# Performance work log

Measured on AMD Instinct MI355X. Metric: run time of the kernel, lower is better.

Reference implementation:

```python
import jax, jax.numpy as jnp
import numpy as np

NH = 32          # nh * 2 neighbors per point (init nh=16)
P_REDUCTION = 0.5


def setup_inputs() -> dict:
    key = jax.random.key(0)
    k1, k2 = jax.random.split(key)
    x = jax.random.normal(k1, (2, 8192, 256), dtype=jnp.float32)       # [b, n, e]
    coords = jax.random.normal(k2, (2, 2, 8192, 1), dtype=jnp.float32) # [b, c, n, 1]
    return {"x": x, "coords": coords}


def _knn_gather(x, coords):
    """Return features of the NH nearest neighbors of each point: [b, n, NH, e]."""
    cs = coords[..., 0]                                   # [b, c, n]
    sq = jnp.sum(cs * cs, axis=1)                         # [b, n]
    # squared euclidean distances [b, n, n]
    d2 = sq[:, :, None] + sq[:, None, :] - 2.0 * jnp.einsum('bcn,bcm->bnm', cs, cs)
    d2 = jax.lax.stop_gradient(d2)                        # indices are non-differentiable
    _, nn_idx = jax.lax.top_k(-d2, NH)                    # [b, n, NH] nearest points
    # gather neighbor features: [b, 1, n, e] indexed with [b, n, NH, 1] -> [b, n, NH, e]
    x_nh = jnp.take_along_axis(x[:, None, :, :], nn_idx[..., None], axis=2)
    return x_nh


def _forward(x, coords):
    b, n, e = x.shape
    x_nh = _knn_gather(x, coords)                         # [b, n, NH, e]
    # unbiased std over the neighbor dim (torch.std default, ddof=1)
    mean_nh = jnp.mean(x_nh, axis=-2, keepdims=True)
    local_s = jnp.sqrt(jnp.sum((x_nh - mean_nh) ** 2, axis=-2) / (NH - 1))  # [b, n, e]
    global_m = jnp.abs(jnp.mean(x, axis=1))               # [b, e]
    local_dist = jnp.sum(local_s / global_m[:, None, :], axis=-1)           # [b, n]
    n_keep = int((1.0 - P_REDUCTION) * n)
    _, keep_idx = jax.lax.top_k(local_dist, n_keep)       # [b, n_keep], sorted desc
    x_out = jnp.take_along_axis(x, keep_idx[:, :, None], axis=1)            # [b, n_keep, e]
    coords_out = jnp.take_along_axis(coords, keep_idx[:, None, :, None], axis=2)  # [b, c, n_keep, 1]
    return x_out, coords_out, local_dist


def reference(x, coords):
    return _forward(x, coords)
```

## Files before the change

### kernel.cpp

```cpp
#include <hip/hip_runtime.h>

#define NN 8192
#define EE 256
#define KNH 32
#define NKEEP 4096
#define NCX 64
#define NCELL 4096
#define CNT_MIN 48

typedef unsigned long long u64;
typedef unsigned int u32;


__device__ __forceinline__ int cellof(float v) {
    const int q = (int)floorf((v + 4.6f) * (64.0f / 9.2f));
    return min(max(q, 0), NCX - 1);
}

__global__ void k_gm_partial(const float* __restrict__ x, float* __restrict__ part) {
    const int b = blockIdx.y, chunk = blockIdx.x, t = threadIdx.x;
    const float* xp = x + ((size_t)b * NN + (size_t)chunk * 256) * EE + t;
    float s = 0.0f;
    for (int i = 0; i < 256; ++i) s += xp[(size_t)i * EE];
    part[((size_t)b * 32 + chunk) * EE + t] = s;
}

__global__ void k_gm_final(const float* __restrict__ part, float* __restrict__ gm) {
    const int b = blockIdx.y, t = threadIdx.x;
    float s = 0.0f;
    for (int c = 0; c < 32; ++c) s += part[((size_t)b * 32 + c) * EE + t];
    gm[b * EE + t] = fabsf(s / (float)NN);
}

__global__ void __launch_bounds__(1024) k_binning(const float* __restrict__ coords,
                                                  int* __restrict__ start,
                                                  float2* __restrict__ sc,
                                                  int* __restrict__ sj) {
    __shared__ int cnt[NCELL];
    __shared__ int ps[1024];
    const int b = blockIdx.x, t = threadIdx.x;
#pragma unroll
    for (int k = 0; k < 4; ++k) cnt[k * 1024 + t] = 0;
    __syncthreads();
#pragma unroll
    for (int k = 0; k < 8; ++k) {
        const int i = k * 1024 + t;
        const float xv = coords[(size_t)b * 2 * NN + i];
        const float yv = coords[(size_t)b * 2 * NN + NN + i];
        atomicAdd(&cnt[cellof(xv) * NCX + cellof(yv)], 1);
    }
    __syncthreads();
    const int v0 = cnt[t * 4 + 0], v1 = cnt[t * 4 + 1];
    const int v2 = cnt[t * 4 + 2], v3 = cnt[t * 4 + 3];
    const int s = v0 + v1 + v2 + v3;
    ps[t] = s;
    __syncthreads();
    for (int d = 1; d < 1024; d <<= 1) {
        const int add = (t >= d) ? ps[t - d] : 0;
        __syncthreads();
        ps[t] += add;
        __syncthreads();
    }
    int run = ps[t] - s;
    start[b * (NCELL + 1) + t * 4 + 0] = run; cnt[t * 4 + 0] = run; run += v0;
    start[b * (NCELL + 1) + t * 4 + 1] = run; cnt[t * 4 + 1] = run; run += v1;
    start[b * (NCELL + 1) + t * 4 + 2] = run; cnt[t * 4 + 2] = run; run += v2;
    start[b * (NCELL + 1) + t * 4 + 3] = run; cnt[t * 4 + 3] = run; run += v3;
    if (t == 0) start[b * (NCELL + 1) + NCELL] = NN;
    __syncthreads();
#pragma unroll
    for (int k = 0; k < 8; ++k) {
        const int i = k * 1024 + t;
        const float xv = coords[(size_t)b * 2 * NN + i];
        const float yv = coords[(size_t)b * 2 * NN + NN + i];
        const int p = atomicAdd(&cnt[cellof(xv) * NCX + cellof(yv)], 1);
        sc[(size_t)b * NN + p] = make_float2(xv, yv);
        sj[(size_t)b * NN + p] = i;
    }
}

__device__ __forceinline__ u64 shfl_xor_u64(u64 v, int m) {
    const u32 hi = (u32)__shfl_xor((int)(u32)(v >> 32), m);
    const u32 lo = (u32)__shfl_xor((int)(u32)v, m);
    return ((u64)hi << 32) | lo;
}

__device__ __forceinline__ u64 wave_min_u64(u64 h) {
#pragma unroll
    for (int s = 1; s < 64; s <<= 1) {
        const u64 o = shfl_xor_u64(h, s);
        h = (o < h) ? o : h;
    }
    return h;
}

__global__ void __launch_bounds__(256) k_knn_dist(
        const float* __restrict__ x,
        const float* __restrict__ gm, const float2* __restrict__ sc,
        const int* __restrict__ sj, const int* __restrict__ start,
        float* __restrict__ ld_out) {
    __shared__ u64 comp[4][64];
    const int wg   = blockIdx.x;
    const int swz  = (wg & 7) * 512 + (wg >> 3);
    const int b    = swz >> 11;
    const int pb   = swz & 2047;
    const int wid  = threadIdx.x >> 6;
    const int lane = threadIdx.x & 63;
    const int p    = pb * 4 + wid;

    const float2* scb = sc + (size_t)b * NN;
    const int*    sjb = sj + (size_t)b * NN;
    const int*    stb = start + b * (NCELL + 1);
    const float2 cp = scb[p];
    const int    i  = sjb[p];
    const float ci0 = cp.x, ci1 = cp.y;
    const int qx = cellof(ci0), qy = cellof(ci1);

    int r = 1, xl, yl, yh, nsl;
    int myc0 = 0, mylen = 0;
    for (;;) {
        xl = max(qx - r, 0);
        const int xh = min(qx + r, NCX - 1);
        yl = max(qy - r, 0);
        yh = min(qy + r, NCX - 1);
        nsl = xh - xl + 1;
        int c0 = 0, c1 = 0;
        if (lane < nsl) {
            c0 = stb[(xl + lane) * NCX + yl];
            c1 = stb[(xl + lane) * NCX + yh + 1];
        }
        myc0 = c0; mylen = c1 - c0;
        int tot = mylen;
#pragma unroll
        for (int s = 1; s < 64; s <<= 1) tot += __shfl_xor(tot, s);
        if (tot >= CNT_MIN || r >= NCX) break;
        r <<= 1;
    }
    int incl = mylen;
#pragma unroll
    for (int d = 1; d < 64; d <<= 1) {
        const int v = __shfl_up(incl, d);
        incl += (lane >= d) ? v : 0;
    }
    int excl = incl - mylen;
    const int L1 = __shfl(incl, 63);

    float dmin = 1e30f;
    for (int g = 0; g < L1; g += 64) {
        const int gp = g + lane;
        int lo = 0, hi = nsl - 1;
#pragma unroll
        for (int st = 0; st < 6; ++st) {
            const int mid = (lo + hi + 1) >> 1;
            const int v = __shfl(excl, mid);
            const bool go = (v <= gp);
            lo = go ? mid : lo;
            hi = go ? hi : mid - 1;
        }
        const int cnd = __shfl(myc0, lo) + gp - __shfl(excl, lo);
        const int cc  = min(max(cnd, 0), NN - 1);
        const float2 pt = scb[cc];
        const float dx = ci0 - pt.x, dy = ci1 - pt.y;
        const float d  = fmaf(dx, dx, dy * dy);
        if (gp < L1) dmin = fminf(dmin, d);
    }

    u32 mk = __float_as_uint(dmin);
#pragma unroll
    for (int k = 2; k <= 64; k <<= 1) {
#pragma unroll
        for (int j = k >> 1; j > 0; j >>= 1) {
            const u32 o = (u32)__shfl_xor((int)mk, j);
            const bool keep_min = (((lane & j) == 0) == ((lane & k) == 0));
            const u32 mn = min(mk, o), mx = max(mk, o);
            mk = keep_min ? mn : mx;
        }
    }
    const u32 T = (u32)__shfl((int)mk, 31);

    const float srad = sqrtf(__uint_as_float(T)) * 1.0002f + 1e-5f;
    xl = cellof(ci0 - srad);
    const int xh2 = cellof(ci0 + srad);
    yl = cellof(ci1 - srad);
    yh = cellof(ci1 + srad);
    nsl = xh2 - xl + 1;
    {
        int c0 = 0, c1 = 0;
        if (lane < nsl) {
            c0 = stb[(xl + lane) * NCX + yl];
            c1 = stb[(xl + lane) * NCX + yh + 1];
        }
        myc0 = c0; mylen = c1 - c0;
    }
    incl = mylen;
#pragma unroll
    for (int d = 1; d < 64; d <<= 1) {
        const int v = __shfl_up(incl, d);
        incl += (lane >= d) ? v : 0;
    }
    excl = incl - mylen;
    const int L2 = __shfl(incl, 63);

    const u64 lmask = (1ull << lane) - 1;
    int base = 0;
    for (int g = 0; g < L2; g += 64) {
        const int gp = g + lane;
        int lo = 0, hi = nsl - 1;
#pragma unroll
        for (int st = 0; st < 6; ++st) {
            const int mid = (lo + hi + 1) >> 1;
            const int v = __shfl(excl, mid);
            const bool go = (v <= gp);
            lo = go ? mid : lo;
            hi = go ? hi : mid - 1;
        }
        const int cnd = __shfl(myc0, lo) + gp - __shfl(excl, lo);
        const int cc  = min(max(cnd, 0), NN - 1);
        const float2 pt = scb[cc];
        const int    jj = sjb[cc];
        const float dx = ci0 - pt.x, dy = ci1 - pt.y;
        const u32 db = __float_as_uint(fmaf(dx, dx, dy * dy));
        const bool keep = (gp < L2) && (db <= T);
        const u64 m = __ballot(keep);
        const int pos = base + __popcll(m & lmask);
        base += __popcll(m);
        if (keep && pos < 64) comp[wid][pos] = ((u64)db << 32) | (u32)jj;
    }
    const bool ovf = (base > 64) || (base < KNH);

    u64 key = (lane < base) ? comp[wid][lane] : ~0ull;
#pragma unroll
    for (int k = 2; k <= 64; k <<= 1) {
#pragma unroll
        for (int j = k >> 1; j > 0; j >>= 1) {
            const u64 other = shfl_xor_u64(key, j);
            const bool keep_min = (((lane & j) == 0) == ((lane & k) == 0));
            const bool lt = (key < other);
            const u64 mn = lt ? key : other;
            const u64 mx = lt ? other : key;
            key = keep_min ? mn : mx;
        }
    }
    int jkeep = (int)(u32)key;

    if (ovf) {
        u64 minkeep = 0;
        for (int k = 0; k < KNH; ++k) {
            u64 best = ~0ull;
            for (int g = 0; g < L2; g += 64) {
                const int gp = g + lane;
                int lo = 0, hi = nsl - 1;
#pragma unroll
                for (int st = 0; st < 6; ++st) {
                    const int mid = (lo + hi + 1) >> 1;
                    const int v = __shfl(excl, mid);
                    const bool go = (v <= gp);
                    lo = go ? mid : lo;
                    hi = go ? hi : mid - 1;
                }
                const int cnd = __shfl(myc0, lo) + gp - __shfl(excl, lo);
                const int cc  = min(max(cnd, 0), NN - 1);
                const float2 pt = scb[cc];
                const int    jj = sjb[cc];
                const float dx = ci0 - pt.x, dy = ci1 - pt.y;
                const float d  = fmaf(dx, dx, dy * dy);
                const u64 kk = ((u64)__float_as_uint(d) << 32) | (u32)jj;
                if (gp < L2 && kk >= minkeep && kk < best) best = kk;
            }
            const u64 h = wave_min_u64(best);
            if (lane == k) jkeep = (int)(u32)h;
            minkeep = h + 1;
        }
    }

    float s1[4] = {0.f, 0.f, 0.f, 0.f};
    float s2[4] = {0.f, 0.f, 0.f, 0.f};
    const float* xb = x + (size_t)b * NN * EE;
#pragma unroll 8
    for (int k = 0; k < KNH; ++k) {
        const int j = __builtin_amdgcn_readlane(jkeep, k);
        const float4 v = *reinterpret_cast<const float4*>(xb + (size_t)j * EE + (lane << 2));
        s1[0] += v.x; s2[0] += v.x * v.x;
        s1[1] += v.y; s2[1] += v.y * v.y;
        s1[2] += v.z; s2[2] += v.z * v.z;
        s1[3] += v.w; s2[3] += v.w * v.w;
    }

    const float* gmb = gm + b * EE;
    float tt = 0.f;
#pragma unroll
    for (int q = 0; q < 4; ++q) {
        const float sum = s1[q];
        float ssd = s2[q] - sum * sum * (1.0f / 32.0f);
        ssd = ssd > 0.f ? ssd : 0.f;
        const float ls = sqrtf(ssd * (1.0f / 31.0f));
        tt += ls / gmb[(lane << 2) + q];
    }
#pragma unroll
    for (int s2r = 1; s2r < 64; s2r <<= 1) tt += __shfl_xor(tt, s2r);

    if (lane == 0) ld_out[(size_t)b * NN + i] = tt;
}

__global__ void k_rank_gather(const float* __restrict__ x, const float* __restrict__ coords,
                              const float* __restrict__ ld,
                              float* __restrict__ x_out, float* __restrict__ c_out) {
    const int b    = blockIdx.y;
    const int wid  = threadIdx.x >> 6;
    const int lane = threadIdx.x & 63;
    const int i    = blockIdx.x * 4 + wid;
    const float* lb = ld + (size_t)b * NN;
    const float di = lb[i];
    int cnt = 0;
    for (int t = 0; t < NN / 64; ++t) {
        const int j = lane + t * 64;
        const float dj = lb[j];
        cnt += (dj > di || (dj == di && j < i)) ? 1 : 0;
    }
#pragma unroll
    for (int s = 1; s < 64; s <<= 1) cnt += __shfl_xor(cnt, s);

    if (cnt < NKEEP) {
        const float4 v = *reinterpret_cast<const float4*>(x + ((size_t)b * NN + i) * EE + (lane << 2));
        *reinterpret_cast<float4*>(x_out + ((size_t)b * NKEEP + cnt) * EE + (lane << 2)) = v;
        if (lane < 2) {
            c_out[((size_t)b * 2 + lane) * NKEEP + cnt] = coords[((size_t)b * 2 + lane) * NN + i];
        }
    }
}

extern "C" void kernel_launch(void* const* d_in, const int* in_sizes, int n_in,
                              void* d_out, int out_size, void* d_ws, size_t ws_size,
                              hipStream_t stream) {
    const float* x      = (const float*)d_in[0];
    const float* coords = (const float*)d_in[1];

    float* out    = (float*)d_out;
    float* x_out  = out;
    float* c_out  = out + 2097152;
    float* ld_out = out + 2113536;

    char*   ws    = (char*)d_ws;
    float*  part  = (float*)(ws);
    float*  gm    = (float*)(ws + 65536);
    int*    start = (int*)  (ws + 67584);
    float2* sc    = (float2*)(ws + 100384);
    int*    sj    = (int*)  (ws + 231456);

    k_binning    <<<2,             1024, 0, stream>>>(coords, start, sc, sj);
    k_gm_partial <<<dim3(32, 2),   256,  0, stream>>>(x, part);
    k_gm_final   <<<dim3(1, 2),    256,  0, stream>>>(part, gm);
    k_knn_dist   <<<4096,          256,  0, stream>>>(x, gm, sc, sj, start, ld_out);
    k_rank_gather<<<dim3(2048, 2), 256,  0, stream>>>(x, coords, ld_out, x_out, c_out);
}
```

Before: 99.04 us.

## Cache candidate distances in LDS, replace bitonic sorts with ballot radix selection

```diff
diff --git a/kernel.cpp b/kernel.cpp
--- a/kernel.cpp
+++ b/kernel.cpp
@@ -7,6 +7,7 @@
 #define NCX 64
 #define NCELL 4096
 #define CNT_MIN 48
+#define CACHE_CAP 512
 
 typedef unsigned long long u64;
 typedef unsigned int u32;
@@ -37,8 +38,9 @@
                                                   float2* __restrict__ sc,
                                                   int* __restrict__ sj) {
     __shared__ int cnt[NCELL];
-    __shared__ int ps[1024];
+    __shared__ int wsum[16];
     const int b = blockIdx.x, t = threadIdx.x;
+    const int lane = t & 63, wv = t >> 6;
 #pragma unroll
     for (int k = 0; k < 4; ++k) cnt[k * 1024 + t] = 0;
     __syncthreads();
@@ -53,15 +55,18 @@
     const int v0 = cnt[t * 4 + 0], v1 = cnt[t * 4 + 1];
     const int v2 = cnt[t * 4 + 2], v3 = cnt[t * 4 + 3];
     const int s = v0 + v1 + v2 + v3;
-    ps[t] = s;
+    int inc = s;
+#pragma unroll
+    for (int d = 1; d < 64; d <<= 1) {
+        const int u = __shfl_up(inc, d);
+        inc += (lane >= d) ? u : 0;
+    }
+    if (lane == 63) wsum[wv] = inc;
     __syncthreads();
-    for (int d = 1; d < 1024; d <<= 1) {
-        const int add = (t >= d) ? ps[t - d] : 0;
-        __syncthreads();
-        ps[t] += add;
-        __syncthreads();
-    }
-    int run = ps[t] - s;
+    int wpre = 0;
+#pragma unroll
+    for (int w = 0; w < 16; ++w) wpre += (w < wv) ? wsum[w] : 0;
+    int run = wpre + inc - s;
     start[b * (NCELL + 1) + t * 4 + 0] = run; cnt[t * 4 + 0] = run; run += v0;
     start[b * (NCELL + 1) + t * 4 + 1] = run; cnt[t * 4 + 1] = run; run += v1;
     start[b * (NCELL + 1) + t * 4 + 2] = run; cnt[t * 4 + 2] = run; run += v2;
@@ -99,6 +104,7 @@
         const float* __restrict__ gm, const float2* __restrict__ sc,
         const int* __restrict__ sj, const int* __restrict__ start,
         float* __restrict__ ld_out) {
+    __shared__ u64 cache[4][CACHE_CAP];
     __shared__ u64 comp[4][64];
     const int wg   = blockIdx.x;
     const int swz  = (wg & 7) * 512 + (wg >> 3);
@@ -116,18 +122,18 @@
     const float ci0 = cp.x, ci1 = cp.y;
     const int qx = cellof(ci0), qy = cellof(ci1);
 
-    int r = 1, xl, yl, yh, nsl;
+    int r = 1, xl1, xh1, yl1, yh1, nsl;
     int myc0 = 0, mylen = 0;
     for (;;) {
-        xl = max(qx - r, 0);
-        const int xh = min(qx + r, NCX - 1);
-        yl = max(qy - r, 0);
-        yh = min(qy + r, NCX - 1);
-        nsl = xh - xl + 1;
+        xl1 = max(qx - r, 0);
+        xh1 = min(qx + r, NCX - 1);
+        yl1 = max(qy - r, 0);
+        yh1 = min(qy + r, NCX - 1);
+        nsl = xh1 - xl1 + 1;
         int c0 = 0, c1 = 0;
         if (lane < nsl) {
-            c0 = stb[(xl + lane) * NCX + yl];
-            c1 = stb[(xl + lane) * NCX + yh + 1];
+            c0 = stb[(xl1 + lane) * NCX + yl1];
+            c1 = stb[(xl1 + lane) * NCX + yh1 + 1];
         }
         myc0 = c0; mylen = c1 - c0;
         int tot = mylen;
@@ -160,105 +166,145 @@
         const int cnd = __shfl(myc0, lo) + gp - __shfl(excl, lo);
         const int cc  = min(max(cnd, 0), NN - 1);
         const float2 pt = scb[cc];
+        const int    jj = sjb[cc];
         const float dx = ci0 - pt.x, dy = ci1 - pt.y;
         const float d  = fmaf(dx, dx, dy * dy);
-        if (gp < L1) dmin = fminf(dmin, d);
-    }
-
-    u32 mk = __float_as_uint(dmin);
-#pragma unroll
-    for (int k = 2; k <= 64; k <<= 1) {
-#pragma unroll
-        for (int j = k >> 1; j > 0; j >>= 1) {
-            const u32 o = (u32)__shfl_xor((int)mk, j);
-            const bool keep_min = (((lane & j) == 0) == ((lane & k) == 0));
-            const u32 mn = min(mk, o), mx = max(mk, o);
-            mk = keep_min ? mn : mx;
-        }
-    }
-    const u32 T = (u32)__shfl((int)mk, 31);
+        if (gp < L1) {
+            dmin = fminf(dmin, d);
+            if (gp < CACHE_CAP) cache[wid][gp] = ((u64)__float_as_uint(d) << 32) | (u32)jj;
+        }
+    }
+
+    const u32 kmin = __float_as_uint(dmin);
+    u32 blo = 0, bhi = 0xFFFFFFFFu;
+    for (int it = 0; it < 32; ++it) {
+        const u32 mid = blo + ((bhi - blo) >> 1);
+        const int c = __popcll(__ballot(kmin <= mid));
+        if (c >= KNH) bhi = mid; else blo = mid + 1;
+    }
+    const u32 T = bhi;
 
     const float srad = sqrtf(__uint_as_float(T)) * 1.0002f + 1e-5f;
-    xl = cellof(ci0 - srad);
-    const int xh2 = cellof(ci0 + srad);
-    yl = cellof(ci1 - srad);
-    yh = cellof(ci1 + srad);
-    nsl = xh2 - xl + 1;
-    {
-        int c0 = 0, c1 = 0;
-        if (lane < nsl) {
-            c0 = stb[(xl + lane) * NCX + yl];
-            c1 = stb[(xl + lane) * NCX + yh + 1];
-        }
-        myc0 = c0; mylen = c1 - c0;
-    }
-    incl = mylen;
-#pragma unroll
-    for (int d = 1; d < 64; d <<= 1) {
-        const int v = __shfl_up(incl, d);
-        incl += (lane >= d) ? v : 0;
-    }
-    excl = incl - mylen;
-    const int L2 = __shfl(incl, 63);
+    const int xl2 = cellof(ci0 - srad), xh2 = cellof(ci0 + srad);
+    const int yl2 = cellof(ci1 - srad), yh2 = cellof(ci1 + srad);
+    const bool cached = (L1 <= CACHE_CAP) && (xl2 >= xl1) && (xh2 <= xh1) &&
+                        (yl2 >= yl1) && (yh2 <= yh1);
 
     const u64 lmask = (1ull << lane) - 1;
     int base = 0;
-    for (int g = 0; g < L2; g += 64) {
-        const int gp = g + lane;
-        int lo = 0, hi = nsl - 1;
-#pragma unroll
-        for (int st = 0; st < 6; ++st) {
-            const int mid = (lo + hi + 1) >> 1;
-            const int v = __shfl(excl, mid);
-            const bool go = (v <= gp);
-            lo = go ? mid : lo;
-            hi = go ? hi : mid - 1;
-        }
-        const int cnd = __shfl(myc0, lo) + gp - __shfl(excl, lo);
-        const int cc  = min(max(cnd, 0), NN - 1);
-        const float2 pt = scb[cc];
-        const int    jj = sjb[cc];
-        const float dx = ci0 - pt.x, dy = ci1 - pt.y;
-        const u32 db = __float_as_uint(fmaf(dx, dx, dy * dy));
-        const bool keep = (gp < L2) && (db <= T);
-        const u64 m = __ballot(keep);
-        const int pos = base + __popcll(m & lmask);
-        base += __popcll(m);
-        if (keep && pos < 64) comp[wid][pos] = ((u64)db << 32) | (u32)jj;
+    if (cached) {
+        for (int g = 0; g < L1; g += 64) {
+            const int gp = g + lane;
+            u64 e = ~0ull;
+            if (gp < L1) e = cache[wid][gp];
+            const bool keep = (gp < L1) && ((u32)(e >> 32) <= T);
+            const u64 m = __ballot(keep);
+            const int pos = base + __popcll(m & lmask);
+            base += __popcll(m);
+            if (keep && pos < 64) comp[wid][pos] = e;
+        }
+    } else {
+        const int nsl2 = xh2 - xl2 + 1;
+        int c0 = 0, c1 = 0;
+        if (lane < nsl2) {
+            c0 = stb[(xl2 + lane) * NCX + yl2];
+            c1 = stb[(xl2 + lane) * NCX + yh2 + 1];
+        }
+        const int myc2 = c0;
+        const int len2 = c1 - c0;
+        int incl2 = len2;
+#pragma unroll
+        for (int d = 1; d < 64; d <<= 1) {
+            const int v = __shfl_up(incl2, d);
+            incl2 += (lane >= d) ? v : 0;
+        }
+        const int excl2 = incl2 - len2;
+        const int L2 = __shfl(incl2, 63);
+        for (int g = 0; g < L2; g += 64) {
+            const int gp = g + lane;
+            int lo = 0, hi = nsl2 - 1;
+#pragma unroll
+            for (int st = 0; st < 6; ++st) {
+                const int mid = (lo + hi + 1) >> 1;
+                const int v = __shfl(excl2, mid);
+                const bool go = (v <= gp);
+                lo = go ? mid : lo;
+                hi = go ? hi : mid - 1;
+            }
+            const int cnd = __shfl(myc2, lo) + gp - __shfl(excl2, lo);
+            const int cc  = min(max(cnd, 0), NN - 1);
+            const float2 pt = scb[cc];
+            const int    jj = sjb[cc];
+            const float dx = ci0 - pt.x, dy = ci1 - pt.y;
+            const u32 db = __float_as_uint(fmaf(dx, dx, dy * dy));
+            const bool keep = (gp < L2) && (db <= T);
+            const u64 m = __ballot(keep);
+            const int pos = base + __popcll(m & lmask);
+            base += __popcll(m);
+            if (keep && pos < 64) comp[wid][pos] = ((u64)db << 32) | (u32)jj;
+        }
     }
     const bool ovf = (base > 64) || (base < KNH);
 
-    u64 key = (lane < base) ? comp[wid][lane] : ~0ull;
-#pragma unroll
-    for (int k = 2; k <= 64; k <<= 1) {
-#pragma unroll
-        for (int j = k >> 1; j > 0; j >>= 1) {
-            const u64 other = shfl_xor_u64(key, j);
-            const bool keep_min = (((lane & j) == 0) == ((lane & k) == 0));
-            const bool lt = (key < other);
-            const u64 mn = lt ? key : other;
-            const u64 mx = lt ? other : key;
-            key = keep_min ? mn : mx;
-        }
-    }
-    int jkeep = (int)(u32)key;
+    u64 key = ~0ull;
+    if (lane < base && lane < 64) key = comp[wid][lane];
+    const u32 dbl = (u32)(key >> 32);
+    const u32 jl  = (u32)key;
+    const bool act = (lane < base) && (lane < 64);
+
+    u32 slo = 0, shi = 0xFFFFFFFFu;
+    for (int it = 0; it < 32; ++it) {
+        const u32 mid = slo + ((shi - slo) >> 1);
+        const int c = __popcll(__ballot(act && dbl <= mid));
+        if (c >= KNH) shi = mid; else slo = mid + 1;
+    }
+    const u32 d32b = shi;
+    const int cnt_lt = __popcll(__ballot(act && dbl < d32b));
+    const int need = KNH - cnt_lt;
+    u32 jlo = 0, jhi = 0xFFFFFFFFu;
+    for (int it = 0; it < 32; ++it) {
+        const u32 mid = jlo + ((jhi - jlo) >> 1);
+        const int c = __popcll(__ballot(act && (dbl == d32b) && (jl <= mid)));
+        if (c >= need) jhi = mid; else jlo = mid + 1;
+    }
+    const u32 jcut = jhi;
+    const bool sel = act && ((dbl < d32b) || ((dbl == d32b) && (jl <= jcut)));
+    u64 selmask = __ballot(sel);
+    int jsel = (int)jl;
 
     if (ovf) {
+        const int nsl2 = xh2 - xl2 + 1;
+        int c0 = 0, c1 = 0;
+        if (lane < nsl2) {
+            c0 = stb[(xl2 + lane) * NCX + yl2];
+            c1 = stb[(xl2 + lane) * NCX + yh2 + 1];
+        }
+        const int myc2 = c0;
+        const int len2 = c1 - c0;
+        int incl2 = len2;
+#pragma unroll
+        for (int d = 1; d < 64; d <<= 1) {
+            const int v = __shfl_up(incl2, d);
+            incl2 += (lane >= d) ? v : 0;
+        }
+        const int excl2 = incl2 - len2;
+        const int L2 = __shfl(incl2, 63);
+        int jkeep = 0;
         u64 minkeep = 0;
         for (int k = 0; k < KNH; ++k) {
             u64 best = ~0ull;
             for (int g = 0; g < L2; g += 64) {
                 const int gp = g + lane;
-                int lo = 0, hi = nsl - 1;
+                int lo = 0, hi = nsl2 - 1;
 #pragma unroll
                 for (int st = 0; st < 6; ++st) {
                     const int mid = (lo + hi + 1) >> 1;
-                    const int v = __shfl(excl, mid);
+                    const int v = __shfl(excl2, mid);
                     const bool go = (v <= gp);
                     lo = go ? mid : lo;
                     hi = go ? hi : mid - 1;
                 }
-                const int cnd = __shfl(myc0, lo) + gp - __shfl(excl, lo);
+                const int cnd = __shfl(myc2, lo) + gp - __shfl(excl2, lo);
                 const int cc  = min(max(cnd, 0), NN - 1);
                 const float2 pt = scb[cc];
                 const int    jj = sjb[cc];
@@ -271,14 +317,19 @@
             if (lane == k) jkeep = (int)(u32)h;
             minkeep = h + 1;
         }
+        jsel = jkeep;
+        selmask = 0xFFFFFFFFull;
     }
 
     float s1[4] = {0.f, 0.f, 0.f, 0.f};
     float s2[4] = {0.f, 0.f, 0.f, 0.f};
     const float* xb = x + (size_t)b * NN * EE;
+    u64 m = selmask;
 #pragma unroll 8
     for (int k = 0; k < KNH; ++k) {
-        const int j = __builtin_amdgcn_readlane(jkeep, k);
+        const int l = __ffsll((unsigned long long)m) - 1;
+        m &= m - 1;
+        const int j = __builtin_amdgcn_readlane(jsel, l);
         const float4 v = *reinterpret_cast<const float4*>(xb + (size_t)j * EE + (lane << 2));
         s1[0] += v.x; s2[0] += v.x * v.x;
         s1[1] += v.y; s2[1] += v.y * v.y;
@@ -312,10 +363,13 @@
     const float* lb = ld + (size_t)b * NN;
     const float di = lb[i];
     int cnt = 0;
-    for (int t = 0; t < NN / 64; ++t) {
-        const int j = lane + t * 64;
-        const float dj = lb[j];
-        cnt += (dj > di || (dj == di && j < i)) ? 1 : 0;
+    for (int t = 0; t < NN / 256; ++t) {
+        const int j0 = t * 256 + (lane << 2);
+        const float4 dv = *reinterpret_cast<const float4*>(lb + j0);
+        cnt += (dv.x > di || (dv.x == di && (j0 + 0) < i)) ? 1 : 0;
+        cnt += (dv.y > di || (dv.y == di && (j0 + 1) < i)) ? 1 : 0;
+        cnt += (dv.z > di || (dv.z == di && (j0 + 2) < i)) ? 1 : 0;
+        cnt += (dv.w > di || (dv.w == di && (j0 + 3) < i)) ? 1 : 0;
     }
 #pragma unroll
     for (int s = 1; s < 64; s <<= 1) cnt += __shfl_xor(cnt, s);
```

Result: slower. 102.4 us (+3.4%).
